# Performance work log

Hardware: AMD Instinct MI355X
Metric: run time of the kernel (lower is better)

The kernel has to match this reference:

```python
import jax, jax.numpy as jnp
import numpy as np

B, T, D, P = 8, 2048, 768, 1024


def setup_inputs() -> dict:
    key = jax.random.key(0)
    kx, kp = jax.random.split(key)
    x = jax.random.normal(kx, (B, T, D), dtype=jnp.float32)
    prototypes = jax.random.normal(kp, (P, D), dtype=jnp.float32)
    return {"x": x, "prototypes": prototypes}


def reference(x, prototypes):
    # sum((x[...,None,:] - p)**2, -1) without the [B,T,P,D] intermediate)
    x_sq = jnp.sum(x * x, axis=-1, keepdims=True)          # [B,T,1]
    p_sq = jnp.sum(prototypes * prototypes, axis=-1)        # [P]
    cross = jnp.einsum("btd,pd->btp", x, prototypes)       # [B,T,P]
    distances = x_sq + p_sq[None, None, :] - 2.0 * cross    # [B,T,P]
    return distances, prototypes
```

## Files before the change

kernel.cpp:

```cpp
#include <hip/hip_runtime.h>
#include <hip/hip_bf16.h>
#include <stdint.h>

#define M_ROWS 16384
#define N_COLS 1024
#define K_DIM  768
#define NKT    12

typedef __attribute__((ext_vector_type(8))) short bf16x8;
typedef __attribute__((ext_vector_type(4))) float f32x4;

__device__ __forceinline__ void async_copy16(void* lds, const void* g) {
  __builtin_amdgcn_global_load_lds(
      (const __attribute__((address_space(1))) unsigned int*)g,
      (__attribute__((address_space(3))) unsigned int*)lds,
      16, 0, 0);
}

__device__ __forceinline__ unsigned short f2bf(float f) {
  __hip_bfloat16 h = __float2bfloat16(f);
  return *reinterpret_cast<unsigned short*>(&h);
}

__global__ void prep_rows(const float* __restrict__ src,
                          unsigned short* __restrict__ dstb,
                          float* __restrict__ sq,
                          float* __restrict__ copy_out) {
  const int wid = threadIdx.x >> 6;
  const int lane = threadIdx.x & 63;
  const int row = blockIdx.x * 4 + wid;
  const float4* r = (const float4*)(src + (size_t)row * K_DIM);
  ushort4* rb = (ushort4*)(dstb + (size_t)row * K_DIM);
  float4* cp = copy_out ? (float4*)(copy_out + (size_t)row * K_DIM) : nullptr;
  float acc = 0.f;
#pragma unroll
  for (int i = 0; i < 3; ++i) {
    float4 v = r[i * 64 + lane];
    acc += v.x * v.x + v.y * v.y + v.z * v.z + v.w * v.w;
    ushort4 u;
    u.x = f2bf(v.x); u.y = f2bf(v.y); u.z = f2bf(v.z); u.w = f2bf(v.w);
    rb[i * 64 + lane] = u;
    if (cp) cp[i * 64 + lane] = v;
  }
#pragma unroll
  for (int off = 32; off; off >>= 1) acc += __shfl_down(acc, off);
  if (lane == 0) sq[row] = acc;
}

__device__ __forceinline__ bf16x8 ldsfrag(const char* tile, int row, int slot) {
  return *(const bf16x8*)(tile + row * 128 + (((slot ^ (row & 7)) << 4)));
}

__global__ __launch_bounds__(512, 2) void dist_gemm(
    const __hip_bfloat16* __restrict__ xb,
    const __hip_bfloat16* __restrict__ pb,
    const float* __restrict__ xsq,
    const float* __restrict__ psq,
    float* __restrict__ out) {
  __shared__ char lds[2][2][32768];

  const int flat = blockIdx.x;
  const int xcd = flat & 7;
  const int local = flat >> 3;
  const int bm = xcd * 8 + (local >> 2);
  const int bn = local & 3;

  const int tid = threadIdx.x;
  const int wave = tid >> 6;
  const int lane = tid & 63;
  const int wm = wave >> 2;
  const int wn = wave & 3;
  const int rl = lane & 15;
  const int kq = lane >> 4;

  f32x4 acc[8][4] = {};
  bf16x8 af[4][2], bfr[4][2];

  const __hip_bfloat16* Abase = xb + (size_t)(bm * 256) * K_DIM;
  const __hip_bfloat16* Bbase = pb + (size_t)(bn * 256) * K_DIM;

  const int rih = tid >> 3;
  const int g8 = (((tid & 7) ^ (rih & 7))) * 8;

#define STAGE(base, tile, h, ktile)                                          \
  do {                                                                       \
    _Pragma("unroll") for (int c = 0; c < 2; ++c) {                          \
      async_copy16((tile) + (h) * 16384 + (c * 512 + tid) * 16,              \
                   (base) + (size_t)((h) * 128 + c * 64 + rih) * K_DIM +     \
                       (ktile) * 64 + g8);                                   \
    }                                                                        \
  } while (0)

  {
    char* A0 = &lds[0][0][0];
    char* B0 = &lds[0][1][0];
    STAGE(Abase, A0, 0, 0);
    STAGE(Abase, A0, 1, 0);
    STAGE(Bbase, B0, 0, 0);
    STAGE(Bbase, B0, 1, 0);
  }
  asm volatile("s_waitcnt vmcnt(0)" ::: "memory");
  asm volatile("s_barrier" ::: "memory");

  for (int kt = 0; kt < NKT; ++kt) {
    const char* At = &lds[kt & 1][0][0];
    const char* Bt = &lds[kt & 1][1][0];
    char* An = &lds[(kt + 1) & 1][0][0];
    char* Bn = &lds[(kt + 1) & 1][1][0];
    const bool pf = (kt + 1 < NKT);

#pragma unroll
    for (int mi = 0; mi < 4; ++mi)
#pragma unroll
      for (int kk = 0; kk < 2; ++kk)
        af[mi][kk] = ldsfrag(At, wm * 128 + mi * 16 + rl, kk * 4 + kq);
#pragma unroll
    for (int ni = 0; ni < 2; ++ni)
#pragma unroll
      for (int kk = 0; kk < 2; ++kk)
        bfr[ni][kk] = ldsfrag(Bt, wn * 64 + ni * 16 + rl, kk * 4 + kq);
    if (pf) STAGE(Abase, An, 0, kt + 1);
    asm volatile("s_barrier" ::: "memory");
    __builtin_amdgcn_s_setprio(1);
#pragma unroll
    for (int mi = 0; mi < 4; ++mi)
#pragma unroll
      for (int ni = 0; ni < 2; ++ni)
#pragma unroll
        for (int kk = 0; kk < 2; ++kk)
          acc[mi][ni] = __builtin_amdgcn_mfma_f32_16x16x32_bf16(
              af[mi][kk], bfr[ni][kk], acc[mi][ni], 0, 0, 0);
    __builtin_amdgcn_s_setprio(0);
    asm volatile("s_barrier" ::: "memory");

#pragma unroll
    for (int ni = 2; ni < 4; ++ni)
#pragma unroll
      for (int kk = 0; kk < 2; ++kk)
        bfr[ni][kk] = ldsfrag(Bt, wn * 64 + ni * 16 + rl, kk * 4 + kq);
    if (pf) STAGE(Abase, An, 1, kt + 1);
    asm volatile("s_barrier" ::: "memory");
    __builtin_amdgcn_s_setprio(1);
#pragma unroll
    for (int mi = 0; mi < 4; ++mi)
#pragma unroll
      for (int ni = 0; ni < 2; ++ni)
#pragma unroll
        for (int kk = 0; kk < 2; ++kk)
          acc[mi][2 + ni] = __builtin_amdgcn_mfma_f32_16x16x32_bf16(
              af[mi][kk], bfr[2 + ni][kk], acc[mi][2 + ni], 0, 0, 0);
    __builtin_amdgcn_s_setprio(0);
    asm volatile("s_barrier" ::: "memory");

#pragma unroll
    for (int mi = 0; mi < 4; ++mi)
#pragma unroll
      for (int kk = 0; kk < 2; ++kk)
        af[mi][kk] = ldsfrag(At, wm * 128 + 64 + mi * 16 + rl, kk * 4 + kq);
    if (pf) STAGE(Bbase, Bn, 0, kt + 1);
    asm volatile("s_barrier" ::: "memory");
    __builtin_amdgcn_s_setprio(1);
#pragma unroll
    for (int mi = 0; mi < 4; ++mi)
#pragma unroll
      for (int ni = 0; ni < 2; ++ni)
#pragma unroll
        for (int kk = 0; kk < 2; ++kk)
          acc[4 + mi][ni] = __builtin_amdgcn_mfma_f32_16x16x32_bf16(
              af[mi][kk], bfr[ni][kk], acc[4 + mi][ni], 0, 0, 0);
    __builtin_amdgcn_s_setprio(0);
    asm volatile("s_barrier" ::: "memory");

    if (pf) STAGE(Bbase, Bn, 1, kt + 1);
    asm volatile("s_barrier" ::: "memory");
    __builtin_amdgcn_s_setprio(1);
#pragma unroll
    for (int mi = 0; mi < 4; ++mi)
#pragma unroll
      for (int ni = 0; ni < 2; ++ni)
#pragma unroll
        for (int kk = 0; kk < 2; ++kk)
          acc[4 + mi][2 + ni] = __builtin_amdgcn_mfma_f32_16x16x32_bf16(
              af[mi][kk], bfr[2 + ni][kk], acc[4 + mi][2 + ni], 0, 0, 0);
    __builtin_amdgcn_s_setprio(0);
    asm volatile("s_waitcnt vmcnt(0)" ::: "memory");
    asm volatile("s_barrier" ::: "memory");
  }
#undef STAGE

  const int r0 = bm * 256 + wm * 128;
  const int c0 = bn * 256 + wn * 64;
#pragma unroll
  for (int mf = 0; mf < 8; ++mf) {
#pragma unroll
    for (int nf = 0; nf < 4; ++nf) {
      const int col = c0 + nf * 16 + rl;
      const float ps = psq[col];
#pragma unroll
      for (int r = 0; r < 4; ++r) {
        const int row = r0 + mf * 16 + kq * 4 + r;
        out[(size_t)row * N_COLS + col] = xsq[row] + ps - 2.0f * acc[mf][nf][r];
      }
    }
  }
}

extern "C" void kernel_launch(void* const* d_in, const int* in_sizes, int n_in,
                              void* d_out, int out_size, void* d_ws, size_t ws_size,
                              hipStream_t stream) {
  const float* x = (const float*)d_in[0];
  const float* p = (const float*)d_in[1];
  float* out = (float*)d_out;
  char* ws = (char*)d_ws;

  float* xsq = (float*)ws;
  float* psq = (float*)(ws + 65536);
  unsigned short* xb = (unsigned short*)(ws + 69632);
  unsigned short* pb = xb + (size_t)M_ROWS * K_DIM;
  float* proto_out = out + (size_t)M_ROWS * N_COLS;

  prep_rows<<<M_ROWS / 4, 256, 0, stream>>>(x, xb, xsq, nullptr);
  prep_rows<<<N_COLS / 4, 256, 0, stream>>>(p, pb, psq, proto_out);

  dist_gemm<<<256, 512, 0, stream>>>((const __hip_bfloat16*)xb,
                                     (const __hip_bfloat16*)pb,
                                     xsq, psq, out);
}
```

Before: 51.98 us.

## Fuse x bf16 conversion and row norms into the GEMM A-tile loading

Drops the separate prep pass over x (a 50MB fp32 read plus a bf16 write, then a bf16 re-read). The GEMM now loads fp32 x directly into registers, converts it to bf16, writes it to swizzled LDS and accumulates per-row squared norms, which are reduced at the end into shared memory. This removes a kernel launch and a large amount of memory traffic. In exchange, A-tile staging becomes synchronous register loads, which adds register pressure and VALU conversion work inside the pipelined main loop.

```diff
diff --git a/kernel.cpp b/kernel.cpp
--- a/kernel.cpp
+++ b/kernel.cpp
@@ -15,6 +15,11 @@
       (const __attribute__((address_space(1))) unsigned int*)g,
       (__attribute__((address_space(3))) unsigned int*)lds,
       16, 0, 0);
+}
+
+__device__ __forceinline__ short b16(float f) {
+  __hip_bfloat16 h = __float2bfloat16(f);
+  return *reinterpret_cast<short*>(&h);
 }
 
 __device__ __forceinline__ unsigned short f2bf(float f) {
@@ -31,7 +36,7 @@
   const int row = blockIdx.x * 4 + wid;
   const float4* r = (const float4*)(src + (size_t)row * K_DIM);
   ushort4* rb = (ushort4*)(dstb + (size_t)row * K_DIM);
-  float4* cp = copy_out ? (float4*)(copy_out + (size_t)row * K_DIM) : nullptr;
+  float4* cp = (float4*)(copy_out + (size_t)row * K_DIM);
   float acc = 0.f;
 #pragma unroll
   for (int i = 0; i < 3; ++i) {
@@ -40,7 +45,7 @@
     ushort4 u;
     u.x = f2bf(v.x); u.y = f2bf(v.y); u.z = f2bf(v.z); u.w = f2bf(v.w);
     rb[i * 64 + lane] = u;
-    if (cp) cp[i * 64 + lane] = v;
+    cp[i * 64 + lane] = v;
   }
 #pragma unroll
   for (int off = 32; off; off >>= 1) acc += __shfl_down(acc, off);
@@ -52,12 +57,12 @@
 }
 
 __global__ __launch_bounds__(512, 2) void dist_gemm(
-    const __hip_bfloat16* __restrict__ xb,
+    const float* __restrict__ x,
     const __hip_bfloat16* __restrict__ pb,
-    const float* __restrict__ xsq,
     const float* __restrict__ psq,
     float* __restrict__ out) {
   __shared__ char lds[2][2][32768];
+  __shared__ float xsq_s[256];
 
   const int flat = blockIdx.x;
   const int xcd = flat & 7;
@@ -75,32 +80,59 @@
 
   f32x4 acc[8][4] = {};
   bf16x8 af[4][2], bfr[4][2];
-
-  const __hip_bfloat16* Abase = xb + (size_t)(bm * 256) * K_DIM;
+  float4 av0[4], av1[4];
+  float ssq[4] = {0.f, 0.f, 0.f, 0.f};
+
+  const float* Ax = x + (size_t)(bm * 256) * K_DIM;
   const __hip_bfloat16* Bbase = pb + (size_t)(bn * 256) * K_DIM;
 
   const int rih = tid >> 3;
-  const int g8 = (((tid & 7) ^ (rih & 7))) * 8;
-
-#define STAGE(base, tile, h, ktile)                                          \
-  do {                                                                       \
-    _Pragma("unroll") for (int c = 0; c < 2; ++c) {                          \
-      async_copy16((tile) + (h) * 16384 + (c * 512 + tid) * 16,              \
-                   (base) + (size_t)((h) * 128 + c * 64 + rih) * K_DIM +     \
-                       (ktile) * 64 + g8);                                   \
-    }                                                                        \
+  const int slot = tid & 7;
+  const int g8 = ((slot ^ (rih & 7))) * 8;
+
+#define ALOAD(ktile)                                                        \
+  do {                                                                      \
+    _Pragma("unroll") for (int g = 0; g < 4; ++g) {                         \
+      const float* ap =                                                     \
+          Ax + (size_t)(g * 64 + rih) * K_DIM + (ktile) * 64 + slot * 8;    \
+      av0[g] = *(const float4*)ap;                                          \
+      av1[g] = *(const float4*)(ap + 4);                                    \
+    }                                                                       \
+  } while (0)
+
+#define AWRITE(tile, g)                                                     \
+  do {                                                                      \
+    const int row_ = (g) * 64 + rih;                                        \
+    bf16x8 v_;                                                              \
+    v_[0] = b16(av0[g].x); v_[1] = b16(av0[g].y);                           \
+    v_[2] = b16(av0[g].z); v_[3] = b16(av0[g].w);                           \
+    v_[4] = b16(av1[g].x); v_[5] = b16(av1[g].y);                           \
+    v_[6] = b16(av1[g].z); v_[7] = b16(av1[g].w);                           \
+    *(bf16x8*)((tile) + row_ * 128 + ((slot ^ (row_ & 7)) << 4)) = v_;      \
+    ssq[g] += av0[g].x * av0[g].x + av0[g].y * av0[g].y +                   \
+              av0[g].z * av0[g].z + av0[g].w * av0[g].w +                   \
+              av1[g].x * av1[g].x + av1[g].y * av1[g].y +                   \
+              av1[g].z * av1[g].z + av1[g].w * av1[g].w;                    \
+  } while (0)
+
+#define BSTAGE(tile, h, ktile)                                              \
+  do {                                                                      \
+    _Pragma("unroll") for (int c = 0; c < 2; ++c) {                         \
+      async_copy16((tile) + (h) * 16384 + (c * 512 + tid) * 16,             \
+                   Bbase + (size_t)((h) * 128 + c * 64 + rih) * K_DIM +     \
+                       (ktile) * 64 + g8);                                  \
+    }                                                                       \
   } while (0)
 
   {
     char* A0 = &lds[0][0][0];
     char* B0 = &lds[0][1][0];
-    STAGE(Abase, A0, 0, 0);
-    STAGE(Abase, A0, 1, 0);
-    STAGE(Bbase, B0, 0, 0);
-    STAGE(Bbase, B0, 1, 0);
-  }
-  asm volatile("s_waitcnt vmcnt(0)" ::: "memory");
-  asm volatile("s_barrier" ::: "memory");
+    BSTAGE(B0, 0, 0);
+    BSTAGE(B0, 1, 0);
+    ALOAD(0);
+    AWRITE(A0, 0); AWRITE(A0, 1); AWRITE(A0, 2); AWRITE(A0, 3);
+  }
+  __syncthreads();
 
   for (int kt = 0; kt < NKT; ++kt) {
     const char* At = &lds[kt & 1][0][0];
@@ -119,7 +151,10 @@
 #pragma unroll
       for (int kk = 0; kk < 2; ++kk)
         bfr[ni][kk] = ldsfrag(Bt, wn * 64 + ni * 16 + rl, kk * 4 + kq);
-    if (pf) STAGE(Abase, An, 0, kt + 1);
+    if (pf) {
+      BSTAGE(Bn, 0, kt + 1);
+      ALOAD(kt + 1);
+    }
     asm volatile("s_barrier" ::: "memory");
     __builtin_amdgcn_s_setprio(1);
 #pragma unroll
@@ -138,7 +173,7 @@
 #pragma unroll
       for (int kk = 0; kk < 2; ++kk)
         bfr[ni][kk] = ldsfrag(Bt, wn * 64 + ni * 16 + rl, kk * 4 + kq);
-    if (pf) STAGE(Abase, An, 1, kt + 1);
+    if (pf) BSTAGE(Bn, 1, kt + 1);
     asm volatile("s_barrier" ::: "memory");
     __builtin_amdgcn_s_setprio(1);
 #pragma unroll
@@ -157,7 +192,7 @@
 #pragma unroll
       for (int kk = 0; kk < 2; ++kk)
         af[mi][kk] = ldsfrag(At, wm * 128 + 64 + mi * 16 + rl, kk * 4 + kq);
-    if (pf) STAGE(Bbase, Bn, 0, kt + 1);
+    if (pf) { AWRITE(An, 0); AWRITE(An, 1); }
     asm volatile("s_barrier" ::: "memory");
     __builtin_amdgcn_s_setprio(1);
 #pragma unroll
@@ -171,7 +206,7 @@
     __builtin_amdgcn_s_setprio(0);
     asm volatile("s_barrier" ::: "memory");
 
-    if (pf) STAGE(Bbase, Bn, 1, kt + 1);
+    if (pf) { AWRITE(An, 2); AWRITE(An, 3); }
     asm volatile("s_barrier" ::: "memory");
     __builtin_amdgcn_s_setprio(1);
 #pragma unroll
@@ -183,12 +218,23 @@
           acc[4 + mi][2 + ni] = __builtin_amdgcn_mfma_f32_16x16x32_bf16(
               af[mi][kk], bfr[2 + ni][kk], acc[4 + mi][2 + ni], 0, 0, 0);
     __builtin_amdgcn_s_setprio(0);
-    asm volatile("s_waitcnt vmcnt(0)" ::: "memory");
-    asm volatile("s_barrier" ::: "memory");
-  }
-#undef STAGE
-
-  const int r0 = bm * 256 + wm * 128;
+    __syncthreads();
+  }
+#undef ALOAD
+#undef AWRITE
+#undef BSTAGE
+
+#pragma unroll
+  for (int g = 0; g < 4; ++g) {
+#pragma unroll
+    for (int m = 1; m < 8; m <<= 1) ssq[g] += __shfl_xor(ssq[g], m);
+  }
+  if (slot == 0) {
+#pragma unroll
+    for (int g = 0; g < 4; ++g) xsq_s[g * 64 + rih] = ssq[g];
+  }
+  __syncthreads();
+
   const int c0 = bn * 256 + wn * 64;
 #pragma unroll
   for (int mf = 0; mf < 8; ++mf) {
@@ -198,8 +244,9 @@
       const float ps = psq[col];
 #pragma unroll
       for (int r = 0; r < 4; ++r) {
-        const int row = r0 + mf * 16 + kq * 4 + r;
-        out[(size_t)row * N_COLS + col] = xsq[row] + ps - 2.0f * acc[mf][nf][r];
+        const int rloc = wm * 128 + mf * 16 + kq * 4 + r;
+        out[(size_t)(bm * 256 + rloc) * N_COLS + col] =
+            xsq_s[rloc] + ps - 2.0f * acc[mf][nf][r];
       }
     }
   }
@@ -213,16 +260,12 @@
   float* out = (float*)d_out;
   char* ws = (char*)d_ws;
 
-  float* xsq = (float*)ws;
-  float* psq = (float*)(ws + 65536);
-  unsigned short* xb = (unsigned short*)(ws + 69632);
-  unsigned short* pb = xb + (size_t)M_ROWS * K_DIM;
+  float* psq = (float*)ws;
+  unsigned short* pbu = (unsigned short*)(ws + 4096);
   float* proto_out = out + (size_t)M_ROWS * N_COLS;
 
-  prep_rows<<<M_ROWS / 4, 256, 0, stream>>>(x, xb, xsq, nullptr);
-  prep_rows<<<N_COLS / 4, 256, 0, stream>>>(p, pb, psq, proto_out);
-
-  dist_gemm<<<256, 512, 0, stream>>>((const __hip_bfloat16*)xb,
-                                     (const __hip_bfloat16*)pb,
-                                     xsq, psq, out);
-}
+  prep_rows<<<N_COLS / 4, 256, 0, stream>>>(p, pbu, psq, proto_out);
+
+  dist_gemm<<<256, 512, 0, stream>>>(x, (const __hip_bfloat16*)pbu,
+                                     psq, out);
+}
```

New measurement: 57.79 us. 1.11x slower.
